# Kernel optimization log

Hardware: AMD Instinct MI355X
Metric: run time of the kernel (lower is better)

## Reference

```python
import jax, jax.numpy as jnp
import numpy as np

L = 2        # num_layers
H = 1024     # hidden_size
S = 2048     # batch_size in the module == number of sequential decode steps


def setup_inputs() -> dict:
    key = jax.random.key(0)
    ks = jax.random.split(key, 8)
    s = 0.02  # small init scale to keep sigmoids/tanh in their linear region

    def init(k, shape, scale=s):
        return jax.random.normal(k, shape, dtype=jnp.float32) * scale

    return {
        "encoder_outputs": init(ks[0], (S, H), 1.0),
        "hidden": jnp.zeros((L, 1, H), jnp.float32),
        "cell": jnp.zeros((L, 1, H), jnp.float32),
        # attn: Linear(2H -> S)
        "attn_w": init(ks[1], (S, 2 * H)), "attn_b": jnp.zeros((S,), jnp.float32),
        # attn_combine: Linear(2H -> H)
        "comb_w": init(ks[2], (H, 2 * H)), "comb_b": jnp.zeros((H,), jnp.float32),
        # LSTM(H, H, num_layers=L); input size == hidden size for every layer
        "w_ih": init(ks[3], (L, 4 * H, H)), "w_hh": init(ks[4], (L, 4 * H, H)),
        "b_ih": jnp.zeros((L, 4 * H), jnp.float32), "b_hh": jnp.zeros((L, 4 * H), jnp.float32),
        # head: Linear(H -> 64) -> ReLU -> Linear(64 -> 2)
        "lin1_w": init(ks[5], (64, H)), "lin1_b": jnp.zeros((64,), jnp.float32),
        "lin2_w": init(ks[6], (2, 64)), "lin2_b": jnp.zeros((2,), jnp.float32),
    }


def reference(encoder_outputs, hidden, cell,
              attn_w, attn_b, comb_w, comb_b,
              w_ih, w_hh, b_ih, b_hh,
              lin1_w, lin1_b, lin2_w, lin2_b):
    n_layers = hidden.shape[0]
    n_steps = encoder_outputs.shape[0]
    h0 = hidden[:, 0, :]   # [L, H]
    c0 = cell[:, 0, :]     # [L, H]
    x0 = jnp.zeros((encoder_outputs.shape[1],), encoder_outputs.dtype)  # decoder_input

    def step(carry, _):
        x, h, c = carry  # x: [H], h/c: [L, H]
        # Bahdanau-style scoring against concat(decoder_input, hidden[0])
        cat1 = jnp.concatenate([x, h[0]])                      # [2H]
        aw = jax.nn.softmax(attn_w @ cat1 + attn_b)            # [S]
        ctx = aw @ encoder_outputs                             # [H]
        inp = jax.nn.relu(comb_w @ jnp.concatenate([x, ctx]) + comb_b)  # [H]
        # one step of a stacked LSTM (PyTorch gate order: i, f, g, o)
        hs, cs = [], []
        for l in range(n_layers):
            gates = w_ih[l] @ inp + b_ih[l] + w_hh[l] @ h[l] + b_hh[l]  # [4H]
            i, f, g, o = jnp.split(gates, 4)
            i = jax.nn.sigmoid(i)
            f = jax.nn.sigmoid(f)
            g = jnp.tanh(g)
            o = jax.nn.sigmoid(o)
            cn = f * c[l] + i * g
            hn = o * jnp.tanh(cn)
            hs.append(hn)
            cs.append(cn)
            inp = hn
        return (inp, jnp.stack(hs), jnp.stack(cs)), inp

    (_, hT, cT), outs = jax.lax.scan(step, (x0, h0, c0), None, length=n_steps)
    # outs: [S, H] -> Linear(H,64) -> ReLU -> Linear(64,2) -> softmax(dim=1)
    hid = jax.nn.relu(outs @ lin1_w.T + lin1_b)
    logits = hid @ lin2_w.T + lin2_b
    probs = jax.nn.softmax(logits, axis=1)
    return probs, hT[:, None, :], cT[:, None, :]
```

## Files before the change

kernel.cpp:

```cpp
#include <hip/hip_runtime.h>
#include <math.h>

#define SD   2048
#define HD   1024
#define TPB  512
#define NBLK 256

#define E_OFF   1024
#define H0_OFF  3072
#define INP_OFF 4096
#define X_OFF   5120
#define M_OFF   8192
#define M_SZ    (HD * SD)
#define XH_OFF  (M_OFF + M_SZ)
#define XH_SZ   ((SD + 1) * HD)
#define WS_NEED_M  ((size_t)(M_OFF + M_SZ + HD) * 4)
#define WS_NEED_XH ((size_t)(XH_OFF + XH_SZ) * 4)

typedef unsigned long long u64;

__device__ __forceinline__ float ldcf(const float* p) {
  return __hip_atomic_load(p, __ATOMIC_RELAXED, __HIP_MEMORY_SCOPE_AGENT);
}
__device__ __forceinline__ float2 ldc2(const float* p) {
  u64 u = __hip_atomic_load((const u64*)p, __ATOMIC_RELAXED, __HIP_MEMORY_SCOPE_AGENT);
  union { u64 u; float2 f; } c; c.u = u; return c.f;
}
__device__ __forceinline__ void stcf(float* p, float v) {
  __hip_atomic_store(p, v, __ATOMIC_RELAXED, __HIP_MEMORY_SCOPE_AGENT);
}
__device__ __forceinline__ unsigned ldb(const unsigned* p) {
  return __hip_atomic_load(p, __ATOMIC_RELAXED, __HIP_MEMORY_SCOPE_AGENT);
}
__device__ __forceinline__ void stb(unsigned* p, unsigned v) {
  __hip_atomic_store(p, v, __ATOMIC_RELAXED, __HIP_MEMORY_SCOPE_AGENT);
}

__device__ __forceinline__ float dot4(float4 a, float4 b) {
  return a.x * b.x + a.y * b.y + a.z * b.z + a.w * b.w;
}
__device__ __forceinline__ float wred(float v) {
  v += __shfl_xor(v, 32, 64); v += __shfl_xor(v, 16, 64);
  v += __shfl_xor(v, 8, 64);  v += __shfl_xor(v, 4, 64);
  v += __shfl_xor(v, 2, 64);  v += __shfl_xor(v, 1, 64);
  return v;
}
__device__ __forceinline__ float sigm(float x) { return 1.0f / (1.0f + __expf(-x)); }

__device__ __forceinline__ void bar_arrive(unsigned* bar, unsigned ep) {
  __syncthreads();
  if (threadIdx.x == 0) stb(bar + blockIdx.x, ep);
}
__device__ __forceinline__ void bar_wait(unsigned* bar, unsigned ep) {
  if (blockIdx.x == 0) {
    if (threadIdx.x < 64) {
      const int lane = threadIdx.x;
      unsigned m;
      do {
        unsigned a = ldb(bar + lane),       b = ldb(bar + 64 + lane);
        unsigned c = ldb(bar + 128 + lane), d = ldb(bar + 192 + lane);
        unsigned ab = a < b ? a : b, cd = c < d ? c : d;
        m = ab < cd ? ab : cd;
#pragma unroll
        for (int s = 32; s; s >>= 1) {
          unsigned o = (unsigned)__shfl_xor((int)m, s, 64);
          m = m < o ? m : o;
        }
      } while (m < ep);
      if (lane < 8) stb(bar + 256 + lane * 16, ep);
    }
  } else if (threadIdx.x == 0) {
    while (ldb(bar + 256 + (blockIdx.x & 7) * 16) < ep)
      __builtin_amdgcn_s_sleep(1);
  }
  __syncthreads();
}

__device__ void classifier8(const float* smx, const float* __restrict__ lin1_w,
                            const float* __restrict__ lin1_b,
                            const float* __restrict__ lin2_w,
                            const float* __restrict__ lin2_b,
                            float* __restrict__ out2, float* scratch) {
  const int tid = threadIdx.x, wid = tid >> 6, lane = tid & 63;
#pragma unroll
  for (int oi = 0; oi < 8; ++oi) {
    const int o = wid * 8 + oi;
    float acc = 0.f;
#pragma unroll
    for (int p = 0; p < 4; ++p)
      acc += dot4(*(const float4*)(lin1_w + (size_t)o * HD + p * 256 + lane * 4),
                  *(const float4*)(smx + p * 256 + lane * 4));
    acc = wred(acc);
    if (lane == 0) scratch[o] = fmaxf(acc + lin1_b[o], 0.f);
  }
  __syncthreads();
  if (tid < 64) {
    float hv = scratch[tid];
    float r0 = wred(hv * lin2_w[tid]);
    float r1 = wred(hv * lin2_w[64 + tid]);
    if (tid == 0) {
      float l0 = r0 + lin2_b[0], l1 = r1 + lin2_b[1];
      float m = fmaxf(l0, l1);
      float e0 = __expf(l0 - m), e1 = __expf(l1 - m);
      float inv = 1.f / (e0 + e1);
      out2[0] = e0 * inv; out2[1] = e1 * inv;
    }
  }
  __syncthreads();
}

template <int MODE>
__global__ void __launch_bounds__(TPB, 2)
decoder_kernel(const float* __restrict__ enc, const float* __restrict__ attn_w,
               const float* __restrict__ attn_b, const float* __restrict__ comb_w,
               const float* __restrict__ comb_b, const float* __restrict__ w_ih,
               const float* __restrict__ w_hh, const float* __restrict__ b_ih,
               const float* __restrict__ b_hh, const float* __restrict__ lin1_w,
               const float* __restrict__ lin1_b, const float* __restrict__ lin2_w,
               const float* __restrict__ lin2_b, const float* __restrict__ hidden,
               const float* __restrict__ cell, float* __restrict__ out,
               float* __restrict__ ws) {
  __shared__ __align__(16) float lds_x[HD];
  __shared__ __align__(16) float lds_h0[HD];
  __shared__ __align__(16) float lds_e[SD];
  __shared__ __align__(16) float lds_v[HD];
  __shared__ __align__(16) float lds_big[8 * HD];
  __shared__ float sg[16], sb[24], bs0[16], bs1[16], scb[4], sc0[4], sc1_[4];

  const int tid = threadIdx.x, wid = tid >> 6, lane = tid & 63;
  const int bid = blockIdx.x;
  unsigned* bar = (unsigned*)ws;
  unsigned ep = 0;

  {
    const int j0 = (bid >> 3) * 32, i0 = (bid & 7) * 256;
    float4 cw0[4], cw1[4], cw2[4], cw3[4];
#pragma unroll
    for (int p = 0; p < 4; ++p) {
      cw0[p] = *(const float4*)(comb_w + (size_t)(j0 + wid * 4 + 0) * 2048 + 1024 + p * 256 + lane * 4);
      cw1[p] = *(const float4*)(comb_w + (size_t)(j0 + wid * 4 + 1) * 2048 + 1024 + p * 256 + lane * 4);
      cw2[p] = *(const float4*)(comb_w + (size_t)(j0 + wid * 4 + 2) * 2048 + 1024 + p * 256 + lane * 4);
      cw3[p] = *(const float4*)(comb_w + (size_t)(j0 + wid * 4 + 3) * 2048 + 1024 + p * 256 + lane * 4);
    }
    for (int ib = 0; ib < 32; ++ib) {
      const int rl = tid >> 6, cs = (tid & 63) * 16;
      const float* src = enc + (size_t)(i0 + ib * 8 + rl) * HD + cs;
#pragma unroll
      for (int q = 0; q < 4; ++q)
        *(float4*)(lds_big + rl * HD + cs + q * 4) = *(const float4*)(src + q * 4);
      __syncthreads();
#pragma unroll 1
      for (int ii = 0; ii < 8; ++ii) {
        float a0 = 0.f, a1 = 0.f, a2 = 0.f, a3 = 0.f;
#pragma unroll
        for (int p = 0; p < 4; ++p) {
          float4 e4 = *(const float4*)(lds_big + ii * HD + p * 256 + lane * 4);
          a0 += dot4(cw0[p], e4); a1 += dot4(cw1[p], e4);
          a2 += dot4(cw2[p], e4); a3 += dot4(cw3[p], e4);
        }
        a0 = wred(a0); a1 = wred(a1); a2 = wred(a2); a3 = wred(a3);
        if (lane == 0) {
          const int i = i0 + ib * 8 + ii;
          stcf(ws + M_OFF + (size_t)(j0 + wid * 4 + 0) * SD + i, a0);
          stcf(ws + M_OFF + (size_t)(j0 + wid * 4 + 1) * SD + i, a1);
          stcf(ws + M_OFF + (size_t)(j0 + wid * 4 + 2) * SD + i, a2);
          stcf(ws + M_OFF + (size_t)(j0 + wid * 4 + 3) * SD + i, a3);
        }
      }
      __syncthreads();
    }
  }
  float* xrow0 = (MODE == 2) ? (ws + XH_OFF) : (ws + X_OFF);
  if (bid == 0) { stcf(xrow0 + tid, 0.f); stcf(xrow0 + 512 + tid, 0.f); }
  *(float2*)(lds_h0 + tid * 2) = *(const float2*)(hidden + tid * 2);
  if (tid < 16) {
    const int kl = tid >> 2, g = tid & 3, k = bid * 4 + kl;
    bs0[tid] = b_ih[g * HD + k] + b_hh[g * HD + k];
    bs1[tid] = b_ih[4 * HD + g * HD + k] + b_hh[4 * HD + g * HD + k];
  }
  if (tid < 4) {
    scb[tid]  = comb_b[bid * 4 + tid];
    sc0[tid]  = cell[bid * 4 + tid];
    sc1_[tid] = cell[HD + bid * 4 + tid];
  }
  ++ep; bar_arrive(bar, ep); bar_wait(bar, ep);

  const int gw = bid * 8 + wid;
  float4 wa[8]; float ab = attn_b[gw];
#pragma unroll
  for (int p = 0; p < 8; ++p)
    wa[p] = *(const float4*)(attn_w + (size_t)gw * 2048 + p * 256 + lane * 4);
  const int jB = bid * 4 + (wid >> 1), half = wid & 1;
  float4 wxp[2], wmp[4];
#pragma unroll
  for (int p = 0; p < 2; ++p)
    wxp[p] = *(const float4*)(comb_w + (size_t)jB * 2048 + half * 512 + p * 256 + lane * 4);
#pragma unroll
  for (int p = 0; p < 4; ++p)
    wmp[p] = *(const float4*)(ws + M_OFF + (size_t)jB * SD + half * 1024 + p * 256 + lane * 4);
  const int kC = bid * 4 + (wid >> 1), gb = (wid & 1) * 2;
  float4 wi0A[4], wi0B[4], wh0A[4], wh0B[4], wi1A[4], wi1B[4], wh1A[4], wh1B[4];
#pragma unroll
  for (int p = 0; p < 4; ++p) {
    wi0A[p] = *(const float4*)(w_ih + (size_t)((gb + 0) * HD + kC) * HD + p * 256 + lane * 4);
    wi0B[p] = *(const float4*)(w_ih + (size_t)((gb + 1) * HD + kC) * HD + p * 256 + lane * 4);
    wh0A[p] = *(const float4*)(w_hh + (size_t)((gb + 0) * HD + kC) * HD + p * 256 + lane * 4);
    wh0B[p] = *(const float4*)(w_hh + (size_t)((gb + 1) * HD + kC) * HD + p * 256 + lane * 4);
    wi1A[p] = *(const float4*)(w_ih + (size_t)4 * HD * HD + (size_t)((gb + 0) * HD + kC) * HD + p * 256 + lane * 4);
    wi1B[p] = *(const float4*)(w_ih + (size_t)4 * HD * HD + (size_t)((gb + 1) * HD + kC) * HD + p * 256 + lane * 4);
    wh1A[p] = *(const float4*)(w_hh + (size_t)4 * HD * HD + (size_t)((gb + 0) * HD + kC) * HD + p * 256 + lane * 4);
    wh1B[p] = *(const float4*)(w_hh + (size_t)4 * HD * HD + (size_t)((gb + 1) * HD + kC) * HD + p * 256 + lane * 4);
  }

  for (int t = 0; t < SD; ++t) {
    const float* xrow_ld = (MODE == 2) ? (ws + XH_OFF + (size_t)t * HD) : (ws + X_OFF);
    float* xrow_st = (MODE == 2) ? (ws + XH_OFF + (size_t)(t + 1) * HD) : (ws + X_OFF);

    *(float2*)(lds_x + tid * 2) = ldc2(xrow_ld + tid * 2);
    __syncthreads();
    {
      float acc = 0.f;
#pragma unroll
      for (int p = 0; p < 4; ++p)
        acc += dot4(wa[p], *(const float4*)(lds_x + p * 256 + lane * 4));
#pragma unroll
      for (int p = 0; p < 4; ++p)
        acc += dot4(wa[4 + p], *(const float4*)(lds_h0 + p * 256 + lane * 4));
      acc = wred(acc);
      if (lane == 0) stcf(ws + E_OFF + gw, __expf(acc + ab));
    }
    ++ep; bar_arrive(bar, ep);
    if (MODE == 1 && bid == NBLK - 1 && t > 0)
      classifier8(lds_x, lin1_w, lin1_b, lin2_w, lin2_b,
                  out + (size_t)(t - 1) * 2, lds_big);
    bar_wait(bar, ep);

    *(float2*)(lds_e + tid * 2)        = ldc2(ws + E_OFF + tid * 2);
    *(float2*)(lds_e + 1024 + tid * 2) = ldc2(ws + E_OFF + 1024 + tid * 2);
    __syncthreads();
    {
      float axh = 0.f, amh = 0.f, esh = 0.f;
#pragma unroll
      for (int p = 0; p < 2; ++p)
        axh += dot4(wxp[p], *(const float4*)(lds_x + half * 512 + p * 256 + lane * 4));
#pragma unroll
      for (int p = 0; p < 4; ++p) {
        float4 e4 = *(const float4*)(lds_e + half * 1024 + p * 256 + lane * 4);
        amh += dot4(wmp[p], e4);
        esh += e4.x + e4.y + e4.z + e4.w;
      }
      axh = wred(axh); amh = wred(amh); esh = wred(esh);
      if (lane == 0) { sb[wid * 3] = axh; sb[wid * 3 + 1] = amh; sb[wid * 3 + 2] = esh; }
    }
    __syncthreads();
    if (tid < 4) {
      float ax = sb[tid * 6] + sb[tid * 6 + 3];
      float am = sb[tid * 6 + 1] + sb[tid * 6 + 4];
      float es = sb[tid * 6 + 2] + sb[tid * 6 + 5];
      stcf(ws + INP_OFF + bid * 4 + tid, fmaxf(ax + am / es + scb[tid], 0.f));
    }
    ++ep; bar_arrive(bar, ep); bar_wait(bar, ep);

    *(float2*)(lds_v + tid * 2) = ldc2(ws + INP_OFF + tid * 2);
    __syncthreads();
    {
      float a0 = 0.f, a1 = 0.f;
#pragma unroll
      for (int p = 0; p < 4; ++p) {
        float4 v4 = *(const float4*)(lds_v + p * 256 + lane * 4);
        float4 h4 = *(const float4*)(lds_h0 + p * 256 + lane * 4);
        a0 += dot4(wi0A[p], v4) + dot4(wh0A[p], h4);
        a1 += dot4(wi0B[p], v4) + dot4(wh0B[p], h4);
      }
      a0 = wred(a0); a1 = wred(a1);
      if (lane == 0) { sg[(wid >> 1) * 4 + gb] = a0; sg[(wid >> 1) * 4 + gb + 1] = a1; }
    }
    __syncthreads();
    if (tid < 4) {
      float gi = sg[tid * 4 + 0] + bs0[tid * 4 + 0];
      float gf = sg[tid * 4 + 1] + bs0[tid * 4 + 1];
      float gg = sg[tid * 4 + 2] + bs0[tid * 4 + 2];
      float go = sg[tid * 4 + 3] + bs0[tid * 4 + 3];
      float c = sigm(gf) * sc0[tid] + sigm(gi) * tanhf(gg);
      sc0[tid] = c;
      stcf(ws + H0_OFF + bid * 4 + tid, sigm(go) * tanhf(c));
    }
    ++ep; bar_arrive(bar, ep); bar_wait(bar, ep);

    *(float2*)(lds_h0 + tid * 2) = ldc2(ws + H0_OFF + tid * 2);
    if (t == 0)
      *(float2*)(lds_x + tid * 2) = *(const float2*)(hidden + HD + tid * 2);
    __syncthreads();
    {
      float a0 = 0.f, a1 = 0.f;
#pragma unroll
      for (int p = 0; p < 4; ++p) {
        float4 v4 = *(const float4*)(lds_h0 + p * 256 + lane * 4);
        float4 h4 = *(const float4*)(lds_x + p * 256 + lane * 4);
        a0 += dot4(wi1A[p], v4) + dot4(wh1A[p], h4);
        a1 += dot4(wi1B[p], v4) + dot4(wh1B[p], h4);
      }
      a0 = wred(a0); a1 = wred(a1);
      if (lane == 0) { sg[(wid >> 1) * 4 + gb] = a0; sg[(wid >> 1) * 4 + gb + 1] = a1; }
    }
    __syncthreads();
    if (tid < 4) {
      float gi = sg[tid * 4 + 0] + bs1[tid * 4 + 0];
      float gf = sg[tid * 4 + 1] + bs1[tid * 4 + 1];
      float gg = sg[tid * 4 + 2] + bs1[tid * 4 + 2];
      float go = sg[tid * 4 + 3] + bs1[tid * 4 + 3];
      float c = sigm(gf) * sc1_[tid] + sigm(gi) * tanhf(gg);
      sc1_[tid] = c;
      stcf(xrow_st + bid * 4 + tid, sigm(go) * tanhf(c));
    }
    ++ep; bar_arrive(bar, ep); bar_wait(bar, ep);
  }

  if (tid < 4) {
    out[4096 + 2 * HD + bid * 4 + tid] = sc0[tid];
    out[4096 + 3 * HD + bid * 4 + tid] = sc1_[tid];
  }
  if (bid == 0) {
    *(float2*)(out + 4096 + tid * 2) = *(const float2*)(lds_h0 + tid * 2);
    const float* xf = (MODE == 2) ? (ws + XH_OFF + (size_t)SD * HD) : (ws + X_OFF);
    float2 x2 = ldc2(xf + tid * 2);
    *(float2*)(out + 4096 + HD + tid * 2) = x2;
  }
  if (MODE == 2) {
    const int tt = bid * 8 + wid;
    const float* xr = ws + XH_OFF + (size_t)(tt + 1) * HD;
    float4 xv[4];
#pragma unroll
    for (int p = 0; p < 4; ++p) xv[p] = *(const float4*)(xr + p * 256 + lane * 4);
    float* hid = lds_big + wid * 64;
#pragma unroll 2
    for (int o = 0; o < 64; ++o) {
      const float* wo = lin1_w + (size_t)o * HD;
      float acc = 0.f;
#pragma unroll
      for (int p = 0; p < 4; ++p)
        acc += dot4(*(const float4*)(wo + p * 256 + lane * 4), xv[p]);
      acc = wred(acc);
      if (lane == 0) hid[o] = fmaxf(acc + lin1_b[o], 0.f);
    }
    float hv = hid[lane];
    float r0 = wred(hv * lin2_w[lane]);
    float r1 = wred(hv * lin2_w[64 + lane]);
    if (lane == 0) {
      float l0 = r0 + lin2_b[0], l1 = r1 + lin2_b[1];
      float m = fmaxf(l0, l1);
      float e0 = __expf(l0 - m), e1 = __expf(l1 - m);
      float inv = 1.f / (e0 + e1);
      out[(size_t)tt * 2]     = e0 * inv;
      out[(size_t)tt * 2 + 1] = e1 * inv;
    }
  } else if (bid == NBLK - 1) {
    *(float2*)(lds_x + tid * 2) = ldc2(ws + X_OFF + tid * 2);
    __syncthreads();
    classifier8(lds_x, lin1_w, lin1_b, lin2_w, lin2_b,
                out + (size_t)(SD - 1) * 2, lds_big);
  }
}

extern "C" void kernel_launch(void* const* d_in, const int* in_sizes, int n_in,
                              void* d_out, int out_size, void* d_ws, size_t ws_size,
                              hipStream_t stream) {
  const float* enc    = (const float*)d_in[0];
  const float* hidden = (const float*)d_in[1];
  const float* cell   = (const float*)d_in[2];
  const float* attn_w = (const float*)d_in[3];
  const float* attn_b = (const float*)d_in[4];
  const float* comb_w = (const float*)d_in[5];
  const float* comb_b = (const float*)d_in[6];
  const float* w_ih   = (const float*)d_in[7];
  const float* w_hh   = (const float*)d_in[8];
  const float* b_ih   = (const float*)d_in[9];
  const float* b_hh   = (const float*)d_in[10];
  const float* lin1_w = (const float*)d_in[11];
  const float* lin1_b = (const float*)d_in[12];
  const float* lin2_w = (const float*)d_in[13];
  const float* lin2_b = (const float*)d_in[14];
  float* out = (float*)d_out;
  float* ws  = (float*)d_ws;

  hipMemsetAsync(d_ws, 0, 4096, stream);
  if (ws_size >= WS_NEED_XH) {
    decoder_kernel<2><<<dim3(NBLK), dim3(TPB), 0, stream>>>(
        enc, attn_w, attn_b, comb_w, comb_b, w_ih, w_hh, b_ih, b_hh,
        lin1_w, lin1_b, lin2_w, lin2_b, hidden, cell, out, ws);
  } else {
    decoder_kernel<1><<<dim3(NBLK), dim3(TPB), 0, stream>>>(
        enc, attn_w, attn_b, comb_w, comb_b, w_ih, w_hh, b_ih, b_hh,
        lin1_w, lin1_b, lin2_w, lin2_b, hidden, cell, out, ws);
  }
  (void)in_sizes; (void)n_in; (void)out_size;
}
```

Before: 23.22 ms.

## Replace per-phase grid barriers with tagged value flags polled by consumers

Each value exchanged between blocks (attention exps, combined input, layer-0 hidden, layer-1 output) is now stored as a 64-bit word that packs the float with a step/phase tag. Consumers spin until all the words they need carry the expected tag, which removes the four grid-wide arrive/wait barriers per decode step. Buffers are double-buffered by step parity to avoid overwrite races, and the full hidden history is written separately for the classifier. This trades barrier latency for more polling traffic and twice the bytes per exchanged value.

```diff
diff --git a/kernel.cpp b/kernel.cpp
--- a/kernel.cpp
+++ b/kernel.cpp
@@ -6,16 +6,15 @@
 #define TPB  512
 #define NBLK 256
 
-#define E_OFF   1024
-#define H0_OFF  3072
-#define INP_OFF 4096
-#define X_OFF   5120
-#define M_OFF   8192
-#define M_SZ    (HD * SD)
-#define XH_OFF  (M_OFF + M_SZ)
-#define XH_SZ   ((SD + 1) * HD)
-#define WS_NEED_M  ((size_t)(M_OFF + M_SZ + HD) * 4)
-#define WS_NEED_XH ((size_t)(XH_OFF + XH_SZ) * 4)
+#define E2_BYTE     4096
+#define INP2_BYTE   (E2_BYTE + 2 * 2048 * 8)
+#define H02_BYTE    (INP2_BYTE + 2 * 1024 * 8)
+#define X2_BYTE     (H02_BYTE + 2 * 1024 * 8)
+#define TAG_END     (X2_BYTE + 2 * 1024 * 8)
+#define M_BYTE      131072
+#define XH_BYTE     (M_BYTE + (size_t)HD * SD * 4)
+#define WS_NEED_M   (M_BYTE + (size_t)HD * SD * 4 + 4096)
+#define WS_NEED_XH  (XH_BYTE + (size_t)(SD + 1) * HD * 4)
 
 typedef unsigned long long u64;
 
@@ -29,11 +28,40 @@
 __device__ __forceinline__ void stcf(float* p, float v) {
   __hip_atomic_store(p, v, __ATOMIC_RELAXED, __HIP_MEMORY_SCOPE_AGENT);
 }
+__device__ __forceinline__ u64 ldc8(const u64* p) {
+  return __hip_atomic_load(p, __ATOMIC_RELAXED, __HIP_MEMORY_SCOPE_AGENT);
+}
+__device__ __forceinline__ void stc8(u64* p, u64 v) {
+  __hip_atomic_store(p, v, __ATOMIC_RELAXED, __HIP_MEMORY_SCOPE_AGENT);
+}
 __device__ __forceinline__ unsigned ldb(const unsigned* p) {
   return __hip_atomic_load(p, __ATOMIC_RELAXED, __HIP_MEMORY_SCOPE_AGENT);
 }
 __device__ __forceinline__ void stb(unsigned* p, unsigned v) {
   __hip_atomic_store(p, v, __ATOMIC_RELAXED, __HIP_MEMORY_SCOPE_AGENT);
+}
+
+__device__ __forceinline__ u64 pk(float v, unsigned tag) {
+  union { float f; unsigned u; } c; c.f = v;
+  return ((u64)tag << 32) | (u64)c.u;
+}
+__device__ __forceinline__ float pv(u64 u) {
+  union { unsigned u; float f; } c; c.u = (unsigned)u; return c.f;
+}
+__device__ __forceinline__ float2 poll2(const u64* p, unsigned T) {
+  u64 a = ldc8(p), b = ldc8(p + 1);
+  while ((unsigned)(a >> 32) < T || (unsigned)(b >> 32) < T) {
+    a = ldc8(p); b = ldc8(p + 1);
+  }
+  float2 r; r.x = pv(a); r.y = pv(b); return r;
+}
+__device__ __forceinline__ float4 poll4(const u64* p, unsigned T) {
+  u64 a = ldc8(p), b = ldc8(p + 1), c = ldc8(p + 2), d = ldc8(p + 3);
+  while ((unsigned)(a >> 32) < T || (unsigned)(b >> 32) < T ||
+         (unsigned)(c >> 32) < T || (unsigned)(d >> 32) < T) {
+    a = ldc8(p); b = ldc8(p + 1); c = ldc8(p + 2); d = ldc8(p + 3);
+  }
+  float4 r; r.x = pv(a); r.y = pv(b); r.z = pv(c); r.w = pv(d); return r;
 }
 
 __device__ __forceinline__ float dot4(float4 a, float4 b) {
@@ -130,7 +158,12 @@
   const int tid = threadIdx.x, wid = tid >> 6, lane = tid & 63;
   const int bid = blockIdx.x;
   unsigned* bar = (unsigned*)ws;
-  unsigned ep = 0;
+  u64* E2   = (u64*)((char*)ws + E2_BYTE);
+  u64* INP2 = (u64*)((char*)ws + INP2_BYTE);
+  u64* H02  = (u64*)((char*)ws + H02_BYTE);
+  u64* X2   = (u64*)((char*)ws + X2_BYTE);
+  float* M  = (float*)((char*)ws + M_BYTE);
+  float* xh = (float*)((char*)ws + XH_BYTE);
 
   {
     const int j0 = (bid >> 3) * 32, i0 = (bid & 7) * 256;
@@ -161,20 +194,18 @@
         a0 = wred(a0); a1 = wred(a1); a2 = wred(a2); a3 = wred(a3);
         if (lane == 0) {
           const int i = i0 + ib * 8 + ii;
-          stcf(ws + M_OFF + (size_t)(j0 + wid * 4 + 0) * SD + i, a0);
-          stcf(ws + M_OFF + (size_t)(j0 + wid * 4 + 1) * SD + i, a1);
-          stcf(ws + M_OFF + (size_t)(j0 + wid * 4 + 2) * SD + i, a2);
-          stcf(ws + M_OFF + (size_t)(j0 + wid * 4 + 3) * SD + i, a3);
+          stcf(M + (size_t)(j0 + wid * 4 + 0) * SD + i, a0);
+          stcf(M + (size_t)(j0 + wid * 4 + 1) * SD + i, a1);
+          stcf(M + (size_t)(j0 + wid * 4 + 2) * SD + i, a2);
+          stcf(M + (size_t)(j0 + wid * 4 + 3) * SD + i, a3);
         }
       }
       __syncthreads();
     }
   }
-  float* xrow0 = (MODE == 2) ? (ws + XH_OFF) : (ws + X_OFF);
-  if (bid == 0) { stcf(xrow0 + tid, 0.f); stcf(xrow0 + 512 + tid, 0.f); }
   *(float2*)(lds_h0 + tid * 2) = *(const float2*)(hidden + tid * 2);
   if (tid < 16) {
-    const int kl = tid >> 2, g = tid & 3, k = bid * 4 + kl;
+    const int g = tid & 3, k = bid * 4 + (tid >> 2);
     bs0[tid] = b_ih[g * HD + k] + b_hh[g * HD + k];
     bs1[tid] = b_ih[4 * HD + g * HD + k] + b_hh[4 * HD + g * HD + k];
   }
@@ -183,7 +214,7 @@
     sc0[tid]  = cell[bid * 4 + tid];
     sc1_[tid] = cell[HD + bid * 4 + tid];
   }
-  ++ep; bar_arrive(bar, ep); bar_wait(bar, ep);
+  bar_arrive(bar, 1); bar_wait(bar, 1);
 
   const int gw = bid * 8 + wid;
   float4 wa[8]; float ab = attn_b[gw];
@@ -197,7 +228,7 @@
     wxp[p] = *(const float4*)(comb_w + (size_t)jB * 2048 + half * 512 + p * 256 + lane * 4);
 #pragma unroll
   for (int p = 0; p < 4; ++p)
-    wmp[p] = *(const float4*)(ws + M_OFF + (size_t)jB * SD + half * 1024 + p * 256 + lane * 4);
+    wmp[p] = *(const float4*)(M + (size_t)jB * SD + half * 1024 + p * 256 + lane * 4);
   const int kC = bid * 4 + (wid >> 1), gb = (wid & 1) * 2;
   float4 wi0A[4], wi0B[4], wh0A[4], wh0B[4], wi1A[4], wi1B[4], wh1A[4], wh1B[4];
 #pragma unroll
@@ -213,10 +244,18 @@
   }
 
   for (int t = 0; t < SD; ++t) {
-    const float* xrow_ld = (MODE == 2) ? (ws + XH_OFF + (size_t)t * HD) : (ws + X_OFF);
-    float* xrow_st = (MODE == 2) ? (ws + XH_OFF + (size_t)(t + 1) * HD) : (ws + X_OFF);
-
-    *(float2*)(lds_x + tid * 2) = ldc2(xrow_ld + tid * 2);
+    const int par = t & 1;
+    const unsigned tb = (unsigned)(t * 4);
+    u64* E2p = E2 + (size_t)par * 2048;
+    u64* I2p = INP2 + (size_t)par * 1024;
+    u64* H2p = H02 + (size_t)par * 1024;
+    u64* X2p = X2 + (size_t)par * 1024;
+    u64* X2n = X2 + (size_t)((t + 1) & 1) * 1024;
+
+    {
+      float2 x2 = poll2(X2p + tid * 2, tb);
+      *(float2*)(lds_x + tid * 2) = x2;
+    }
     __syncthreads();
     {
       float acc = 0.f;
@@ -227,16 +266,16 @@
       for (int p = 0; p < 4; ++p)
         acc += dot4(wa[4 + p], *(const float4*)(lds_h0 + p * 256 + lane * 4));
       acc = wred(acc);
-      if (lane == 0) stcf(ws + E_OFF + gw, __expf(acc + ab));
-    }
-    ++ep; bar_arrive(bar, ep);
+      if (lane == 0) stc8(E2p + gw, pk(__expf(acc + ab), tb + 1));
+    }
     if (MODE == 1 && bid == NBLK - 1 && t > 0)
       classifier8(lds_x, lin1_w, lin1_b, lin2_w, lin2_b,
                   out + (size_t)(t - 1) * 2, lds_big);
-    bar_wait(bar, ep);
-
-    *(float2*)(lds_e + tid * 2)        = ldc2(ws + E_OFF + tid * 2);
-    *(float2*)(lds_e + 1024 + tid * 2) = ldc2(ws + E_OFF + 1024 + tid * 2);
+
+    {
+      float4 e4 = poll4(E2p + tid * 4, tb + 1);
+      *(float4*)(lds_e + tid * 4) = e4;
+    }
     __syncthreads();
     {
       float axh = 0.f, amh = 0.f, esh = 0.f;
@@ -257,11 +296,13 @@
       float ax = sb[tid * 6] + sb[tid * 6 + 3];
       float am = sb[tid * 6 + 1] + sb[tid * 6 + 4];
       float es = sb[tid * 6 + 2] + sb[tid * 6 + 5];
-      stcf(ws + INP_OFF + bid * 4 + tid, fmaxf(ax + am / es + scb[tid], 0.f));
-    }
-    ++ep; bar_arrive(bar, ep); bar_wait(bar, ep);
-
-    *(float2*)(lds_v + tid * 2) = ldc2(ws + INP_OFF + tid * 2);
+      stc8(I2p + bid * 4 + tid, pk(fmaxf(ax + am / es + scb[tid], 0.f), tb + 2));
+    }
+
+    {
+      float2 v2 = poll2(I2p + tid * 2, tb + 2);
+      *(float2*)(lds_v + tid * 2) = v2;
+    }
     __syncthreads();
     {
       float a0 = 0.f, a1 = 0.f;
@@ -283,13 +324,15 @@
       float go = sg[tid * 4 + 3] + bs0[tid * 4 + 3];
       float c = sigm(gf) * sc0[tid] + sigm(gi) * tanhf(gg);
       sc0[tid] = c;
-      stcf(ws + H0_OFF + bid * 4 + tid, sigm(go) * tanhf(c));
-    }
-    ++ep; bar_arrive(bar, ep); bar_wait(bar, ep);
-
-    *(float2*)(lds_h0 + tid * 2) = ldc2(ws + H0_OFF + tid * 2);
-    if (t == 0)
-      *(float2*)(lds_x + tid * 2) = *(const float2*)(hidden + HD + tid * 2);
+      stc8(H2p + bid * 4 + tid, pk(sigm(go) * tanhf(c), tb + 3));
+    }
+
+    {
+      float2 h2 = poll2(H2p + tid * 2, tb + 3);
+      *(float2*)(lds_h0 + tid * 2) = h2;
+      if (t == 0)
+        *(float2*)(lds_x + tid * 2) = *(const float2*)(hidden + HD + tid * 2);
+    }
     __syncthreads();
     {
       float a0 = 0.f, a1 = 0.f;
@@ -311,35 +354,39 @@
       float go = sg[tid * 4 + 3] + bs1[tid * 4 + 3];
       float c = sigm(gf) * sc1_[tid] + sigm(gi) * tanhf(gg);
       sc1_[tid] = c;
-      stcf(xrow_st + bid * 4 + tid, sigm(go) * tanhf(c));
-    }
-    ++ep; bar_arrive(bar, ep); bar_wait(bar, ep);
-  }
-
+      float h1v = sigm(go) * tanhf(c);
+      stc8(X2n + bid * 4 + tid, pk(h1v, tb + 4));
+      if (MODE == 2) stcf(xh + (size_t)(t + 1) * HD + bid * 4 + tid, h1v);
+    }
+  }
+
+  bar_arrive(bar, 2); bar_wait(bar, 2);
   if (tid < 4) {
     out[4096 + 2 * HD + bid * 4 + tid] = sc0[tid];
     out[4096 + 3 * HD + bid * 4 + tid] = sc1_[tid];
   }
   if (bid == 0) {
     *(float2*)(out + 4096 + tid * 2) = *(const float2*)(lds_h0 + tid * 2);
-    const float* xf = (MODE == 2) ? (ws + XH_OFF + (size_t)SD * HD) : (ws + X_OFF);
-    float2 x2 = ldc2(xf + tid * 2);
-    *(float2*)(out + 4096 + HD + tid * 2) = x2;
+    const u64* xf = X2 + (size_t)(SD & 1) * 1024;
+    out[4096 + HD + tid]       = pv(ldc8(xf + tid));
+    out[4096 + HD + 512 + tid] = pv(ldc8(xf + 512 + tid));
   }
   if (MODE == 2) {
     const int tt = bid * 8 + wid;
-    const float* xr = ws + XH_OFF + (size_t)(tt + 1) * HD;
-    float4 xv[4];
-#pragma unroll
-    for (int p = 0; p < 4; ++p) xv[p] = *(const float4*)(xr + p * 256 + lane * 4);
+    const float* xr = xh + (size_t)(tt + 1) * HD;
+    float2 xv2[8];
+#pragma unroll
+    for (int p = 0; p < 8; ++p) xv2[p] = ldc2(xr + p * 128 + lane * 2);
     float* hid = lds_big + wid * 64;
 #pragma unroll 2
     for (int o = 0; o < 64; ++o) {
       const float* wo = lin1_w + (size_t)o * HD;
       float acc = 0.f;
 #pragma unroll
-      for (int p = 0; p < 4; ++p)
-        acc += dot4(*(const float4*)(wo + p * 256 + lane * 4), xv[p]);
+      for (int p = 0; p < 8; ++p) {
+        float2 w2 = *(const float2*)(wo + p * 128 + lane * 2);
+        acc += w2.x * xv2[p].x + w2.y * xv2[p].y;
+      }
       acc = wred(acc);
       if (lane == 0) hid[o] = fmaxf(acc + lin1_b[o], 0.f);
     }
@@ -355,7 +402,9 @@
       out[(size_t)tt * 2 + 1] = e1 * inv;
     }
   } else if (bid == NBLK - 1) {
-    *(float2*)(lds_x + tid * 2) = ldc2(ws + X_OFF + tid * 2);
+    const u64* xf = X2 + (size_t)(SD & 1) * 1024;
+    lds_x[tid]       = pv(ldc8(xf + tid));
+    lds_x[512 + tid] = pv(ldc8(xf + 512 + tid));
     __syncthreads();
     classifier8(lds_x, lin1_w, lin1_b, lin2_w, lin2_b,
                 out + (size_t)(SD - 1) * 2, lds_big);
@@ -383,7 +432,7 @@
   float* out = (float*)d_out;
   float* ws  = (float*)d_ws;
 
-  hipMemsetAsync(d_ws, 0, 4096, stream);
+  hipMemsetAsync(d_ws, 0, TAG_END, stream);
   if (ws_size >= WS_NEED_XH) {
     decoder_kernel<2><<<dim3(NBLK), dim3(TPB), 0, stream>>>(
         enc, attn_w, attn_b, comb_w, comb_b, w_ih, w_hh, b_ih, b_hh,
```

After: 31.53 ms. 35.8% more time.

## Decentralize grid barrier polling and fuse stage loads into barrier wait

Applied to the files above, without the earlier changes.

Replaces the two-level grid barrier, where block 0 aggregated arrivals and broadcast a release flag, with a scheme where every block's first wavefront polls all 256 arrival counters directly. The same wavefront then copies the next stage's vector from global workspace into LDS, which removes a separate load-plus-syncthreads round. The combine stage is also restructured so each wave pair computes a full output row redundantly rather than splitting halves through shared memory and an extra syncthreads. The aim is lower per-step barrier latency; the cost is heavier polling traffic on the counters and the copy being done by only 64 threads per block.

```diff
diff --git a/kernel.cpp b/kernel.cpp
--- a/kernel.cpp
+++ b/kernel.cpp
@@ -51,27 +51,25 @@
   __syncthreads();
   if (threadIdx.x == 0) stb(bar + blockIdx.x, ep);
 }
-__device__ __forceinline__ void bar_wait(unsigned* bar, unsigned ep) {
-  if (blockIdx.x == 0) {
-    if (threadIdx.x < 64) {
-      const int lane = threadIdx.x;
-      unsigned m;
-      do {
-        unsigned a = ldb(bar + lane),       b = ldb(bar + 64 + lane);
-        unsigned c = ldb(bar + 128 + lane), d = ldb(bar + 192 + lane);
-        unsigned ab = a < b ? a : b, cd = c < d ? c : d;
-        m = ab < cd ? ab : cd;
-#pragma unroll
-        for (int s = 32; s; s >>= 1) {
-          unsigned o = (unsigned)__shfl_xor((int)m, s, 64);
-          m = m < o ? m : o;
-        }
-      } while (m < ep);
-      if (lane < 8) stb(bar + 256 + lane * 16, ep);
-    }
-  } else if (threadIdx.x == 0) {
-    while (ldb(bar + 256 + (blockIdx.x & 7) * 16) < ep)
-      __builtin_amdgcn_s_sleep(1);
+__device__ __forceinline__ void bar_wait_stage(unsigned* bar, unsigned ep,
+                                               float* d0, const float* s0, int n0) {
+  if (threadIdx.x < 64) {
+    const int lane = threadIdx.x;
+    unsigned m;
+    do {
+      unsigned a = ldb(bar + lane),       b = ldb(bar + 64 + lane);
+      unsigned c = ldb(bar + 128 + lane), d = ldb(bar + 192 + lane);
+      unsigned ab = a < b ? a : b, cd = c < d ? c : d;
+      m = ab < cd ? ab : cd;
+#pragma unroll
+      for (int s = 32; s; s >>= 1) {
+        unsigned o = (unsigned)__shfl_xor((int)m, s, 64);
+        m = m < o ? m : o;
+      }
+    } while (m < ep);
+    if (d0)
+      for (int i = lane; i < n0; i += 64)
+        *(float2*)(d0 + 2 * i) = ldc2(s0 + 2 * i);
   }
   __syncthreads();
 }
@@ -125,7 +123,7 @@
   __shared__ __align__(16) float lds_e[SD];
   __shared__ __align__(16) float lds_v[HD];
   __shared__ __align__(16) float lds_big[8 * HD];
-  __shared__ float sg[16], sb[24], bs0[16], bs1[16], scb[4], sc0[4], sc1_[4];
+  __shared__ float sg[16], bs0[16], bs1[16], scb[4], sc0[4], sc1_[4];
 
   const int tid = threadIdx.x, wid = tid >> 6, lane = tid & 63;
   const int bid = blockIdx.x;
@@ -174,7 +172,7 @@
   if (bid == 0) { stcf(xrow0 + tid, 0.f); stcf(xrow0 + 512 + tid, 0.f); }
   *(float2*)(lds_h0 + tid * 2) = *(const float2*)(hidden + tid * 2);
   if (tid < 16) {
-    const int kl = tid >> 2, g = tid & 3, k = bid * 4 + kl;
+    const int g = tid & 3, k = bid * 4 + (tid >> 2);
     bs0[tid] = b_ih[g * HD + k] + b_hh[g * HD + k];
     bs1[tid] = b_ih[4 * HD + g * HD + k] + b_hh[4 * HD + g * HD + k];
   }
@@ -183,21 +181,22 @@
     sc0[tid]  = cell[bid * 4 + tid];
     sc1_[tid] = cell[HD + bid * 4 + tid];
   }
-  ++ep; bar_arrive(bar, ep); bar_wait(bar, ep);
+  ++ep; bar_arrive(bar, ep);
+  bar_wait_stage(bar, ep, nullptr, nullptr, 0);
 
   const int gw = bid * 8 + wid;
   float4 wa[8]; float ab = attn_b[gw];
 #pragma unroll
   for (int p = 0; p < 8; ++p)
     wa[p] = *(const float4*)(attn_w + (size_t)gw * 2048 + p * 256 + lane * 4);
-  const int jB = bid * 4 + (wid >> 1), half = wid & 1;
-  float4 wxp[2], wmp[4];
-#pragma unroll
-  for (int p = 0; p < 2; ++p)
-    wxp[p] = *(const float4*)(comb_w + (size_t)jB * 2048 + half * 512 + p * 256 + lane * 4);
+  const int jB = bid * 4 + (wid >> 1);
+  float4 wxp[4], wmp[8];
 #pragma unroll
   for (int p = 0; p < 4; ++p)
-    wmp[p] = *(const float4*)(ws + M_OFF + (size_t)jB * SD + half * 1024 + p * 256 + lane * 4);
+    wxp[p] = *(const float4*)(comb_w + (size_t)jB * 2048 + p * 256 + lane * 4);
+#pragma unroll
+  for (int p = 0; p < 8; ++p)
+    wmp[p] = *(const float4*)(ws + M_OFF + (size_t)jB * SD + p * 256 + lane * 4);
   const int kC = bid * 4 + (wid >> 1), gb = (wid & 1) * 2;
   float4 wi0A[4], wi0B[4], wh0A[4], wh0B[4], wi1A[4], wi1B[4], wh1A[4], wh1B[4];
 #pragma unroll
@@ -216,8 +215,7 @@
     const float* xrow_ld = (MODE == 2) ? (ws + XH_OFF + (size_t)t * HD) : (ws + X_OFF);
     float* xrow_st = (MODE == 2) ? (ws + XH_OFF + (size_t)(t + 1) * HD) : (ws + X_OFF);
 
-    *(float2*)(lds_x + tid * 2) = ldc2(xrow_ld + tid * 2);
-    __syncthreads();
+    bar_wait_stage(bar, ep, lds_x, xrow_ld, 512);
     {
       float acc = 0.f;
 #pragma unroll
@@ -233,36 +231,26 @@
     if (MODE == 1 && bid == NBLK - 1 && t > 0)
       classifier8(lds_x, lin1_w, lin1_b, lin2_w, lin2_b,
                   out + (size_t)(t - 1) * 2, lds_big);
-    bar_wait(bar, ep);
-
-    *(float2*)(lds_e + tid * 2)        = ldc2(ws + E_OFF + tid * 2);
-    *(float2*)(lds_e + 1024 + tid * 2) = ldc2(ws + E_OFF + 1024 + tid * 2);
-    __syncthreads();
+
+    bar_wait_stage(bar, ep, lds_e, ws + E_OFF, 1024);
     {
-      float axh = 0.f, amh = 0.f, esh = 0.f;
-#pragma unroll
-      for (int p = 0; p < 2; ++p)
-        axh += dot4(wxp[p], *(const float4*)(lds_x + half * 512 + p * 256 + lane * 4));
-#pragma unroll
-      for (int p = 0; p < 4; ++p) {
-        float4 e4 = *(const float4*)(lds_e + half * 1024 + p * 256 + lane * 4);
-        amh += dot4(wmp[p], e4);
-        esh += e4.x + e4.y + e4.z + e4.w;
-      }
-      axh = wred(axh); amh = wred(amh); esh = wred(esh);
-      if (lane == 0) { sb[wid * 3] = axh; sb[wid * 3 + 1] = amh; sb[wid * 3 + 2] = esh; }
-    }
-    __syncthreads();
-    if (tid < 4) {
-      float ax = sb[tid * 6] + sb[tid * 6 + 3];
-      float am = sb[tid * 6 + 1] + sb[tid * 6 + 4];
-      float es = sb[tid * 6 + 2] + sb[tid * 6 + 5];
-      stcf(ws + INP_OFF + bid * 4 + tid, fmaxf(ax + am / es + scb[tid], 0.f));
-    }
-    ++ep; bar_arrive(bar, ep); bar_wait(bar, ep);
-
-    *(float2*)(lds_v + tid * 2) = ldc2(ws + INP_OFF + tid * 2);
-    __syncthreads();
+      float ax = 0.f, am = 0.f, es = 0.f;
+#pragma unroll
+      for (int p = 0; p < 4; ++p)
+        ax += dot4(wxp[p], *(const float4*)(lds_x + p * 256 + lane * 4));
+#pragma unroll
+      for (int p = 0; p < 8; ++p) {
+        float4 e4 = *(const float4*)(lds_e + p * 256 + lane * 4);
+        am += dot4(wmp[p], e4);
+        es += e4.x + e4.y + e4.z + e4.w;
+      }
+      ax = wred(ax); am = wred(am); es = wred(es);
+      if ((wid & 1) == 0 && lane == 0)
+        stcf(ws + INP_OFF + jB, fmaxf(ax + am / es + scb[wid >> 1], 0.f));
+    }
+    ++ep; bar_arrive(bar, ep);
+
+    bar_wait_stage(bar, ep, lds_v, ws + INP_OFF, 512);
     {
       float a0 = 0.f, a1 = 0.f;
 #pragma unroll
@@ -285,12 +273,13 @@
       sc0[tid] = c;
       stcf(ws + H0_OFF + bid * 4 + tid, sigm(go) * tanhf(c));
     }
-    ++ep; bar_arrive(bar, ep); bar_wait(bar, ep);
-
-    *(float2*)(lds_h0 + tid * 2) = ldc2(ws + H0_OFF + tid * 2);
-    if (t == 0)
+    ++ep; bar_arrive(bar, ep);
+
+    bar_wait_stage(bar, ep, lds_h0, ws + H0_OFF, 512);
+    if (t == 0) {
       *(float2*)(lds_x + tid * 2) = *(const float2*)(hidden + HD + tid * 2);
-    __syncthreads();
+      __syncthreads();
+    }
     {
       float a0 = 0.f, a1 = 0.f;
 #pragma unroll
@@ -313,9 +302,10 @@
       sc1_[tid] = c;
       stcf(xrow_st + bid * 4 + tid, sigm(go) * tanhf(c));
     }
-    ++ep; bar_arrive(bar, ep); bar_wait(bar, ep);
-  }
-
+    ++ep; bar_arrive(bar, ep);
+  }
+
+  bar_wait_stage(bar, ep, nullptr, nullptr, 0);
   if (tid < 4) {
     out[4096 + 2 * HD + bid * 4 + tid] = sc0[tid];
     out[4096 + 3 * HD + bid * 4 + tid] = sc1_[tid];
@@ -331,7 +321,11 @@
     const float* xr = ws + XH_OFF + (size_t)(tt + 1) * HD;
     float4 xv[4];
 #pragma unroll
-    for (int p = 0; p < 4; ++p) xv[p] = *(const float4*)(xr + p * 256 + lane * 4);
+    for (int p = 0; p < 4; ++p) {
+      float2 lo = ldc2(xr + p * 256 + lane * 4);
+      float2 hi = ldc2(xr + p * 256 + lane * 4 + 2);
+      xv[p].x = lo.x; xv[p].y = lo.y; xv[p].z = hi.x; xv[p].w = hi.y;
+    }
     float* hid = lds_big + wid * 64;
 #pragma unroll 2
     for (int o = 0; o < 64; ++o) {
```

Result: slower. 64.39 ms (+177.4%).

## Give each wave full gate rows to drop intra-block LDS reductions and syncs

Applied to the files above, without the earlier changes.

Changes the per-block work split so each wave owns one full output row. Waves 0-3 handle attn_combine and layer-0 LSTM rows, waves 4-7 handle layer-1 rows, and each wave computes all four gates and applies the cell update in registers. This removes the shared-memory partial-sum exchange and two __syncthreads per stage in the latency-bound sequential loop. The cost is that half the waves sit idle in each stage, with longer per-wave dot products. The final classifier also switches its x-row loads to coherent loads.

```diff
diff --git a/kernel.cpp b/kernel.cpp
--- a/kernel.cpp
+++ b/kernel.cpp
@@ -125,7 +125,6 @@
   __shared__ __align__(16) float lds_e[SD];
   __shared__ __align__(16) float lds_v[HD];
   __shared__ __align__(16) float lds_big[8 * HD];
-  __shared__ float sg[16], sb[24], bs0[16], bs1[16], scb[4], sc0[4], sc1_[4];
 
   const int tid = threadIdx.x, wid = tid >> 6, lane = tid & 63;
   const int bid = blockIdx.x;
@@ -173,16 +172,16 @@
   float* xrow0 = (MODE == 2) ? (ws + XH_OFF) : (ws + X_OFF);
   if (bid == 0) { stcf(xrow0 + tid, 0.f); stcf(xrow0 + 512 + tid, 0.f); }
   *(float2*)(lds_h0 + tid * 2) = *(const float2*)(hidden + tid * 2);
-  if (tid < 16) {
-    const int kl = tid >> 2, g = tid & 3, k = bid * 4 + kl;
-    bs0[tid] = b_ih[g * HD + k] + b_hh[g * HD + k];
-    bs1[tid] = b_ih[4 * HD + g * HD + k] + b_hh[4 * HD + g * HD + k];
-  }
-  if (tid < 4) {
-    scb[tid]  = comb_b[bid * 4 + tid];
-    sc0[tid]  = cell[bid * 4 + tid];
-    sc1_[tid] = cell[HD + bid * 4 + tid];
-  }
+
+  const int kRow = bid * 4 + (wid & 3);
+  const int bOff = (wid < 4) ? 0 : 4 * HD;
+  float bsg0 = b_ih[bOff + kRow]          + b_hh[bOff + kRow];
+  float bsg1 = b_ih[bOff + HD + kRow]     + b_hh[bOff + HD + kRow];
+  float bsg2 = b_ih[bOff + 2 * HD + kRow] + b_hh[bOff + 2 * HD + kRow];
+  float bsg3 = b_ih[bOff + 3 * HD + kRow] + b_hh[bOff + 3 * HD + kRow];
+  float crow = cell[(wid < 4 ? 0 : HD) + kRow];
+  float scbw = (wid < 4) ? comb_b[kRow] : 0.f;
+
   ++ep; bar_arrive(bar, ep); bar_wait(bar, ep);
 
   const int gw = bid * 8 + wid;
@@ -190,26 +189,27 @@
 #pragma unroll
   for (int p = 0; p < 8; ++p)
     wa[p] = *(const float4*)(attn_w + (size_t)gw * 2048 + p * 256 + lane * 4);
-  const int jB = bid * 4 + (wid >> 1), half = wid & 1;
-  float4 wxp[2], wmp[4];
-#pragma unroll
-  for (int p = 0; p < 2; ++p)
-    wxp[p] = *(const float4*)(comb_w + (size_t)jB * 2048 + half * 512 + p * 256 + lane * 4);
-#pragma unroll
-  for (int p = 0; p < 4; ++p)
-    wmp[p] = *(const float4*)(ws + M_OFF + (size_t)jB * SD + half * 1024 + p * 256 + lane * 4);
-  const int kC = bid * 4 + (wid >> 1), gb = (wid & 1) * 2;
-  float4 wi0A[4], wi0B[4], wh0A[4], wh0B[4], wi1A[4], wi1B[4], wh1A[4], wh1B[4];
-#pragma unroll
-  for (int p = 0; p < 4; ++p) {
-    wi0A[p] = *(const float4*)(w_ih + (size_t)((gb + 0) * HD + kC) * HD + p * 256 + lane * 4);
-    wi0B[p] = *(const float4*)(w_ih + (size_t)((gb + 1) * HD + kC) * HD + p * 256 + lane * 4);
-    wh0A[p] = *(const float4*)(w_hh + (size_t)((gb + 0) * HD + kC) * HD + p * 256 + lane * 4);
-    wh0B[p] = *(const float4*)(w_hh + (size_t)((gb + 1) * HD + kC) * HD + p * 256 + lane * 4);
-    wi1A[p] = *(const float4*)(w_ih + (size_t)4 * HD * HD + (size_t)((gb + 0) * HD + kC) * HD + p * 256 + lane * 4);
-    wi1B[p] = *(const float4*)(w_ih + (size_t)4 * HD * HD + (size_t)((gb + 1) * HD + kC) * HD + p * 256 + lane * 4);
-    wh1A[p] = *(const float4*)(w_hh + (size_t)4 * HD * HD + (size_t)((gb + 0) * HD + kC) * HD + p * 256 + lane * 4);
-    wh1B[p] = *(const float4*)(w_hh + (size_t)4 * HD * HD + (size_t)((gb + 1) * HD + kC) * HD + p * 256 + lane * 4);
+
+  float4 wxp[4], wmp[8];
+  if (wid < 4) {
+#pragma unroll
+    for (int p = 0; p < 4; ++p)
+      wxp[p] = *(const float4*)(comb_w + (size_t)kRow * 2048 + p * 256 + lane * 4);
+#pragma unroll
+    for (int p = 0; p < 8; ++p)
+      wmp[p] = *(const float4*)(ws + M_OFF + (size_t)kRow * SD + p * 256 + lane * 4);
+  }
+  float4 wi[4][4], wh[4][4];
+  {
+    const float* wiB = w_ih + (size_t)bOff * HD;
+    const float* whB = w_hh + (size_t)bOff * HD;
+#pragma unroll
+    for (int g = 0; g < 4; ++g)
+#pragma unroll
+      for (int p = 0; p < 4; ++p) {
+        wi[g][p] = *(const float4*)(wiB + (size_t)(g * HD + kRow) * HD + p * 256 + lane * 4);
+        wh[g][p] = *(const float4*)(whB + (size_t)(g * HD + kRow) * HD + p * 256 + lane * 4);
+      }
   }
 
   for (int t = 0; t < SD; ++t) {
@@ -238,52 +238,41 @@
     *(float2*)(lds_e + tid * 2)        = ldc2(ws + E_OFF + tid * 2);
     *(float2*)(lds_e + 1024 + tid * 2) = ldc2(ws + E_OFF + 1024 + tid * 2);
     __syncthreads();
-    {
-      float axh = 0.f, amh = 0.f, esh = 0.f;
-#pragma unroll
-      for (int p = 0; p < 2; ++p)
-        axh += dot4(wxp[p], *(const float4*)(lds_x + half * 512 + p * 256 + lane * 4));
-#pragma unroll
-      for (int p = 0; p < 4; ++p) {
-        float4 e4 = *(const float4*)(lds_e + half * 1024 + p * 256 + lane * 4);
-        amh += dot4(wmp[p], e4);
-        esh += e4.x + e4.y + e4.z + e4.w;
-      }
-      axh = wred(axh); amh = wred(amh); esh = wred(esh);
-      if (lane == 0) { sb[wid * 3] = axh; sb[wid * 3 + 1] = amh; sb[wid * 3 + 2] = esh; }
-    }
-    __syncthreads();
-    if (tid < 4) {
-      float ax = sb[tid * 6] + sb[tid * 6 + 3];
-      float am = sb[tid * 6 + 1] + sb[tid * 6 + 4];
-      float es = sb[tid * 6 + 2] + sb[tid * 6 + 5];
-      stcf(ws + INP_OFF + bid * 4 + tid, fmaxf(ax + am / es + scb[tid], 0.f));
+    if (wid < 4) {
+      float ax = 0.f, am = 0.f, es = 0.f;
+#pragma unroll
+      for (int p = 0; p < 4; ++p)
+        ax += dot4(wxp[p], *(const float4*)(lds_x + p * 256 + lane * 4));
+#pragma unroll
+      for (int p = 0; p < 8; ++p) {
+        float4 e4 = *(const float4*)(lds_e + p * 256 + lane * 4);
+        am += dot4(wmp[p], e4);
+        es += e4.x + e4.y + e4.z + e4.w;
+      }
+      ax = wred(ax); am = wred(am); es = wred(es);
+      if (lane == 0) stcf(ws + INP_OFF + kRow, fmaxf(ax + am / es + scbw, 0.f));
     }
     ++ep; bar_arrive(bar, ep); bar_wait(bar, ep);
 
     *(float2*)(lds_v + tid * 2) = ldc2(ws + INP_OFF + tid * 2);
     __syncthreads();
-    {
-      float a0 = 0.f, a1 = 0.f;
+    if (wid < 4) {
+      float a0 = 0.f, a1 = 0.f, a2 = 0.f, a3 = 0.f;
 #pragma unroll
       for (int p = 0; p < 4; ++p) {
         float4 v4 = *(const float4*)(lds_v + p * 256 + lane * 4);
         float4 h4 = *(const float4*)(lds_h0 + p * 256 + lane * 4);
-        a0 += dot4(wi0A[p], v4) + dot4(wh0A[p], h4);
-        a1 += dot4(wi0B[p], v4) + dot4(wh0B[p], h4);
-      }
-      a0 = wred(a0); a1 = wred(a1);
-      if (lane == 0) { sg[(wid >> 1) * 4 + gb] = a0; sg[(wid >> 1) * 4 + gb + 1] = a1; }
-    }
-    __syncthreads();
-    if (tid < 4) {
-      float gi = sg[tid * 4 + 0] + bs0[tid * 4 + 0];
-      float gf = sg[tid * 4 + 1] + bs0[tid * 4 + 1];
-      float gg = sg[tid * 4 + 2] + bs0[tid * 4 + 2];
-      float go = sg[tid * 4 + 3] + bs0[tid * 4 + 3];
-      float c = sigm(gf) * sc0[tid] + sigm(gi) * tanhf(gg);
-      sc0[tid] = c;
-      stcf(ws + H0_OFF + bid * 4 + tid, sigm(go) * tanhf(c));
+        a0 += dot4(wi[0][p], v4) + dot4(wh[0][p], h4);
+        a1 += dot4(wi[1][p], v4) + dot4(wh[1][p], h4);
+        a2 += dot4(wi[2][p], v4) + dot4(wh[2][p], h4);
+        a3 += dot4(wi[3][p], v4) + dot4(wh[3][p], h4);
+      }
+      a0 = wred(a0); a1 = wred(a1); a2 = wred(a2); a3 = wred(a3);
+      if (lane == 0) {
+        float c = sigm(a1 + bsg1) * crow + sigm(a0 + bsg0) * tanhf(a2 + bsg2);
+        crow = c;
+        stcf(ws + H0_OFF + kRow, sigm(a3 + bsg3) * tanhf(c));
+      }
     }
     ++ep; bar_arrive(bar, ep); bar_wait(bar, ep);
 
@@ -291,35 +280,31 @@
     if (t == 0)
       *(float2*)(lds_x + tid * 2) = *(const float2*)(hidden + HD + tid * 2);
     __syncthreads();
-    {
-      float a0 = 0.f, a1 = 0.f;
+    if (wid >= 4) {
+      float a0 = 0.f, a1 = 0.f, a2 = 0.f, a3 = 0.f;
 #pragma unroll
       for (int p = 0; p < 4; ++p) {
         float4 v4 = *(const float4*)(lds_h0 + p * 256 + lane * 4);
         float4 h4 = *(const float4*)(lds_x + p * 256 + lane * 4);
-        a0 += dot4(wi1A[p], v4) + dot4(wh1A[p], h4);
-        a1 += dot4(wi1B[p], v4) + dot4(wh1B[p], h4);
-      }
-      a0 = wred(a0); a1 = wred(a1);
-      if (lane == 0) { sg[(wid >> 1) * 4 + gb] = a0; sg[(wid >> 1) * 4 + gb + 1] = a1; }
-    }
-    __syncthreads();
-    if (tid < 4) {
-      float gi = sg[tid * 4 + 0] + bs1[tid * 4 + 0];
-      float gf = sg[tid * 4 + 1] + bs1[tid * 4 + 1];
-      float gg = sg[tid * 4 + 2] + bs1[tid * 4 + 2];
-      float go = sg[tid * 4 + 3] + bs1[tid * 4 + 3];
-      float c = sigm(gf) * sc1_[tid] + sigm(gi) * tanhf(gg);
-      sc1_[tid] = c;
-      stcf(xrow_st + bid * 4 + tid, sigm(go) * tanhf(c));
+        a0 += dot4(wi[0][p], v4) + dot4(wh[0][p], h4);
+        a1 += dot4(wi[1][p], v4) + dot4(wh[1][p], h4);
+        a2 += dot4(wi[2][p], v4) + dot4(wh[2][p], h4);
+        a3 += dot4(wi[3][p], v4) + dot4(wh[3][p], h4);
+      }
+      a0 = wred(a0); a1 = wred(a1); a2 = wred(a2); a3 = wred(a3);
+      if (lane == 0) {
+        float c = sigm(a1 + bsg1) * crow + sigm(a0 + bsg0) * tanhf(a2 + bsg2);
+        crow = c;
+        float h1v = sigm(a3 + bsg3) * tanhf(c);
+        stcf(xrow_st + kRow, h1v);
+        if (MODE == 2 && t == SD - 1) {  }
+      }
     }
     ++ep; bar_arrive(bar, ep); bar_wait(bar, ep);
   }
 
-  if (tid < 4) {
-    out[4096 + 2 * HD + bid * 4 + tid] = sc0[tid];
-    out[4096 + 3 * HD + bid * 4 + tid] = sc1_[tid];
-  }
+  if (lane == 0)
+    out[4096 + (wid < 4 ? 2 * HD : 3 * HD) + kRow] = crow;
   if (bid == 0) {
     *(float2*)(out + 4096 + tid * 2) = *(const float2*)(lds_h0 + tid * 2);
     const float* xf = (MODE == 2) ? (ws + XH_OFF + (size_t)SD * HD) : (ws + X_OFF);
@@ -331,7 +316,11 @@
     const float* xr = ws + XH_OFF + (size_t)(tt + 1) * HD;
     float4 xv[4];
 #pragma unroll
-    for (int p = 0; p < 4; ++p) xv[p] = *(const float4*)(xr + p * 256 + lane * 4);
+    for (int p = 0; p < 4; ++p) {
+      float2 lo = ldc2(xr + p * 256 + lane * 4);
+      float2 hi = ldc2(xr + p * 256 + lane * 4 + 2);
+      xv[p].x = lo.x; xv[p].y = lo.y; xv[p].z = hi.x; xv[p].w = hi.y;
+    }
     float* hid = lds_big + wid * 64;
 #pragma unroll 2
     for (int o = 0; o < 64; ++o) {
```

Measured after the change: 31.25 ms. 34.6% more time.
